# Optimization experiments

Measured on AMD Instinct MI355X. Metric: run time of the kernel, lower is better.

## Reference

```python
import jax, jax.numpy as jnp
import numpy as np

N_NODES = 100000
N_EDGES = 1600000
F_IN = 128
HID = 128  # nhid*2
NHID = 64
N_GRAPHS = 512
N_CLASSES = 10
NEG_SLOPE = 0.2  # PyG GATConv default


def setup_inputs() -> dict:
    key = jax.random.key(0)
    ks = jax.random.split(key, 16)
    x = jax.random.normal(ks[0], (N_NODES, F_IN), dtype=jnp.float32)
    edge_index = jax.random.randint(ks[1], (2, N_EDGES), 0, N_NODES, dtype=jnp.int64)
    batch = jnp.sort(jax.random.randint(ks[2], (N_NODES,), 0, N_GRAPHS, dtype=jnp.int64))
    def lin(k, fan_in, shape):
        bound = 1.0 / np.sqrt(fan_in)
        return jax.random.uniform(k, shape, jnp.float32, -bound, bound)
    return {
        "x": x, "edge_index": edge_index, "batch": batch,
        "W1": lin(ks[3], F_IN, (F_IN, HID)),
        "a_src1": lin(ks[4], HID, (HID,)),
        "a_dst1": lin(ks[5], HID, (HID,)),
        "b1": jnp.zeros((HID,), jnp.float32),
        "W2": lin(ks[6], HID, (HID, HID)),
        "a_src2": lin(ks[7], HID, (HID,)),
        "a_dst2": lin(ks[8], HID, (HID,)),
        "b2": jnp.zeros((HID,), jnp.float32),
        "W_fc1": lin(ks[9], HID, (HID, NHID)),
        "b_fc1": lin(ks[10], HID, (NHID,)),
        "W_fc2": lin(ks[11], NHID, (NHID, N_CLASSES)),
        "b_fc2": lin(ks[12], NHID, (N_CLASSES,)),
    }


def gat_conv(x, src, dst, W, a_src, a_dst, b):
    # h = W x ; attention e_ij = LeakyReLU(a_src.h_i + a_dst.h_j), softmax over
    # incoming edges of each destination j, then scatter-add aggregation.
    h = x @ W                                   # [N, H]
    alpha_s = h @ a_src                         # [N]
    alpha_d = h @ a_dst                         # [N]
    e = jax.nn.leaky_relu(alpha_s[src] + alpha_d[dst], NEG_SLOPE)  # [E]
    n = x.shape[0]
    m = jax.ops.segment_max(e, dst, num_segments=n)                # per-dst max
    ex = jnp.exp(e - m[dst])
    denom = jax.ops.segment_sum(ex, dst, num_segments=n)
    alpha = ex / denom[dst]                                        # [E]
    out = jax.ops.segment_sum(alpha[:, None] * h[src], dst, num_segments=n)
    return out + b


def reference(x, edge_index, batch, W1, a_src1, a_dst1, b1,
              W2, a_src2, a_dst2, b2, W_fc1, b_fc1, W_fc2, b_fc2):
    n = x.shape[0]
    # GATConv default add_self_loops=True
    loops = jnp.arange(n, dtype=edge_index.dtype)
    src = jnp.concatenate([edge_index[0], loops])
    dst = jnp.concatenate([edge_index[1], loops])

    h = jax.nn.selu(gat_conv(x, src, dst, W1, a_src1, a_dst1, b1))
    h = jax.nn.selu(gat_conv(h, src, dst, W2, a_src2, a_dst2, b2))

    # global mean pool over graphs
    sums = jax.ops.segment_sum(h, batch, num_segments=N_GRAPHS)
    cnts = jax.ops.segment_sum(jnp.ones((n,), h.dtype), batch, num_segments=N_GRAPHS)
    pooled = jax.nn.selu(sums / jnp.maximum(cnts, 1.0)[:, None])   # [G, H]

    g = jax.nn.selu(pooled @ W_fc1 + b_fc1)
    # dropout p=0.5 is identity in eval mode
    logits = g @ W_fc2 + b_fc2
    return jax.nn.log_softmax(logits, axis=-1)
```

## Files before the change

### kernel.cpp

```cpp
#include <hip/hip_runtime.h>
#include <hip/hip_bf16.h>

#define NEG_SLOPE 0.2f
typedef unsigned int uint32;

#define BSHIFT 9
#define BSIZE 512
#define MAXB 256
#define PCHUNK 2048
#define PEPT 8
#define BSTRIDE 12288

typedef __attribute__((ext_vector_type(8))) __bf16 bf16x8;
typedef __attribute__((ext_vector_type(4))) float f32x4;
typedef __attribute__((ext_vector_type(2))) float f32x2;

__device__ __forceinline__ float selu_f(float x) {
    const float a = 1.6732632423543772f, s = 1.0507009873554805f;
    return x > 0.0f ? s * x : s * a * (__expf(x) - 1.0f);
}

__device__ __forceinline__ unsigned short f2bf(float x) {
    uint32 u = __float_as_uint(x);
    uint32 r = (u + 0x7fff + ((u >> 16) & 1)) >> 16;
    return (unsigned short)r;
}
__device__ __forceinline__ float bf_lo(uint32 g) { return __uint_as_float(g << 16); }
__device__ __forceinline__ float bf_hi(uint32 g) { return __uint_as_float(g & 0xffff0000u); }

__global__ __launch_bounds__(256) void prep9(const float* __restrict__ W1,
                                             const float* __restrict__ W2,
                                             unsigned short* __restrict__ Wb,
                                             const int* __restrict__ batch,
                                             int* __restrict__ gstart,
                                             int N, int G) {
    int b = blockIdx.x, t = threadIdx.x;
    if (b < 2) {
        const float* W = b ? W2 : W1;
        unsigned short* oh = Wb + (size_t)b * 32768;
        unsigned short* ol = oh + 16384;
        for (int d = t; d < 16384; d += 256) {
            int j = d & 7, nn = (d >> 3) & 127, g = d >> 10;
            float v = W[(g * 8 + j) * 128 + nn];
            uint32 hu = f2bf(v);
            float hv = __uint_as_float(hu << 16);
            oh[d] = (unsigned short)hu;
            ol[d] = f2bf(v - hv);
        }
    } else {
        int i = (b - 2) * 256 + t;
        if (i < N) {
            int bb = batch[i];
            int bp = (i == 0) ? -1 : batch[i - 1];
            for (int q = bp + 1; q <= bb; ++q) gstart[q] = i;
            if (i == N - 1)
                for (int q = bb + 1; q <= G; ++q) gstart[q] = N;
        }
    }
}

__global__ __launch_bounds__(256) void partition_edges(const int* __restrict__ ei,
                                                       int* __restrict__ gcur0,
                                                       uint32* __restrict__ tmp,
                                                       int E, int TOT) {
    __shared__ int lcnt[MAXB];
    __shared__ int lstart[MAXB];
    __shared__ int lcur[MAXB];
    __shared__ int gbase[MAXB];
    __shared__ uint32 staged[PCHUNK];
    __shared__ unsigned char bslot[PCHUNK];
    int t = threadIdx.x;
    int eb = blockIdx.x * PCHUNK;
    int sreg[PEPT], dreg[PEPT];
    #pragma unroll
    for (int k = 0; k < PEPT; ++k) {
        int e = eb + k * 256 + t;
        if (e < TOT) {
            if (e < E) { sreg[k] = ei[e]; dreg[k] = ei[E + e]; }
            else       { sreg[k] = dreg[k] = e - E; }
        } else dreg[k] = -1;
    }
    lcnt[t] = 0;
    __syncthreads();
    #pragma unroll
    for (int k = 0; k < PEPT; ++k)
        if (dreg[k] >= 0) atomicAdd(&lcnt[dreg[k] >> BSHIFT], 1);
    __syncthreads();
    int v = lcnt[t];
    lstart[t] = v;
    __syncthreads();
    for (int off = 1; off < 256; off <<= 1) {
        int add = (t >= off) ? lstart[t - off] : 0;
        __syncthreads();
        lstart[t] += add;
        __syncthreads();
    }
    int ex = lstart[t] - v;
    __syncthreads();
    lstart[t] = ex;
    lcur[t] = ex;
    if (v > 0) gbase[t] = t * BSTRIDE + atomicAdd(&gcur0[t], v);
    __syncthreads();
    #pragma unroll
    for (int k = 0; k < PEPT; ++k) {
        int d = dreg[k];
        if (d >= 0) {
            int b = d >> BSHIFT;
            int p = atomicAdd(&lcur[b], 1);
            staged[p] = ((uint32)(d & (BSIZE - 1)) << 17) | (uint32)sreg[k];
            bslot[p] = (unsigned char)b;
        }
    }
    __syncthreads();
    int nvalid = TOT - eb; if (nvalid > PCHUNK) nvalid = PCHUNK;
    for (int i = t; i < nvalid; i += 256) {
        int b = bslot[i];
        tmp[gbase[b] + (i - lstart[b])] = staged[i];
    }
}

__global__ __launch_bounds__(1024) void bucket_build(const uint32* __restrict__ tmp,
                                                     const int* __restrict__ gcur0,
                                                     int* __restrict__ rowptr,
                                                     int* __restrict__ rowend,
                                                     int* __restrict__ col,
                                                     int N, int NB) {
    __shared__ int cnt[BSIZE];
    __shared__ int sums[256];
    int b = blockIdx.x, t = threadIdx.x;
    int lo = b << BSHIFT;
    int nn = N - lo; if (nn > BSIZE) nn = BSIZE;
    if (t < BSIZE) cnt[t] = 0;
    __syncthreads();
    int ebeg = b * BSTRIDE;
    int eend = ebeg + gcur0[b];
    for (int i = ebeg + t; i < eend; i += 1024)
        atomicAdd(&cnt[tmp[i] >> 17], 1);
    __syncthreads();
    int c0 = 0, c1 = 0, s2 = 0;
    if (t < 256) {
        c0 = cnt[2 * t]; c1 = cnt[2 * t + 1];
        s2 = c0 + c1;
        sums[t] = s2;
    }
    __syncthreads();
    for (int off = 1; off < 256; off <<= 1) {
        int add = (t < 256 && t >= off) ? sums[t - off] : 0;
        __syncthreads();
        if (t < 256) sums[t] += add;
        __syncthreads();
    }
    if (t < 256) {
        int ex = sums[t] - s2;
        int st0 = ebeg + ex, st1 = st0 + c0;
        if (2 * t < nn)     { rowptr[lo + 2 * t] = st0;     rowend[lo + 2 * t] = st0 + c0; }
        if (2 * t + 1 < nn) { rowptr[lo + 2 * t + 1] = st1; rowend[lo + 2 * t + 1] = st1 + c1; }
        cnt[2 * t] = st0; cnt[2 * t + 1] = st1;
    }
    __syncthreads();
    for (int i = ebeg + t; i < eend; i += 1024) {
        uint32 u = tmp[i];
        int p = atomicAdd(&cnt[u >> 17], 1);
        col[p] = (int)(u & 0x1FFFFu);
    }
}

__device__ __forceinline__ void gemm_core(const bf16x8 ah[2][4],
                                          const __bf16* Wl,
                                          const float* a_src, const float* a_dst,
                                          uint32* hb, float* as_, float* ad_,
                                          int rbase, int n, int col16, int quad) {
    f32x4 acc[2][8];
    #pragma unroll
    for (int mt = 0; mt < 2; ++mt)
        #pragma unroll
        for (int t = 0; t < 8; ++t) acc[mt][t] = (f32x4)(0.0f);

    #pragma unroll
    for (int c = 0; c < 4; ++c) {
        #pragma unroll
        for (int t = 0; t < 8; ++t) {
            int off = (((c * 4 + quad) * 128) + t * 16 + col16) * 8;
            bf16x8 bh = *(const bf16x8*)&Wl[off];
            bf16x8 bl = *(const bf16x8*)&Wl[16384 + off];
            #pragma unroll
            for (int mt = 0; mt < 2; ++mt) {
                acc[mt][t] = __builtin_amdgcn_mfma_f32_16x16x32_bf16(ah[mt][c], bh, acc[mt][t], 0, 0, 0);
                acc[mt][t] = __builtin_amdgcn_mfma_f32_16x16x32_bf16(ah[mt][c], bl, acc[mt][t], 0, 0, 0);
            }
        }
    }
    float asv[8], adv[8];
    #pragma unroll
    for (int t = 0; t < 8; ++t) { asv[t] = a_src[t * 16 + col16]; adv[t] = a_dst[t * 16 + col16]; }
    #pragma unroll
    for (int mt = 0; mt < 2; ++mt) {
        #pragma unroll
        for (int reg = 0; reg < 4; ++reg) {
            float s = 0.0f, d = 0.0f;
            #pragma unroll
            for (int t = 0; t < 8; ++t) {
                float v = acc[mt][t][reg];
                s += v * asv[t]; d += v * adv[t];
            }
            #pragma unroll
            for (int off = 1; off < 16; off <<= 1) {
                s += __shfl_xor(s, off);
                d += __shfl_xor(d, off);
            }
            int r = rbase + mt * 16 + quad * 4 + reg;
            if (col16 == 0 && r < n) { as_[r] = s; ad_[r] = d; }
        }
    }
    #pragma unroll
    for (int mt = 0; mt < 2; ++mt)
    #pragma unroll
    for (int t = 0; t < 8; ++t)
    #pragma unroll
    for (int reg = 0; reg < 4; ++reg) {
        float v = acc[mt][t][reg];
        float p = __shfl_xor(v, 1);
        int r = rbase + mt * 16 + quad * 4 + reg;
        if (!(col16 & 1) && r < n) {
            uint32 pk = (uint32)f2bf(v) | ((uint32)f2bf(p) << 16);
            hb[(size_t)r * 64 + t * 8 + (col16 >> 1)] = pk;
        }
    }
}

__global__ __launch_bounds__(256) void gemm_mfma_f32(const float* __restrict__ X,
                                                     const unsigned short* __restrict__ Wbh,
                                                     const float* __restrict__ a_src,
                                                     const float* __restrict__ a_dst,
                                                     uint32* __restrict__ hb,
                                                     float* __restrict__ as_,
                                                     float* __restrict__ ad_, int n) {
    __shared__ __bf16 Wl[32768];
    const int tid = threadIdx.x;
    {
        const uint4* sw = (const uint4*)Wbh;
        uint4* dw = (uint4*)Wl;
        for (int i = tid; i < 4096; i += 256) dw[i] = sw[i];
    }
    const int lane = tid & 63, wid = tid >> 6;
    const int col16 = lane & 15, quad = lane >> 4;
    const int rbase = blockIdx.x * 128 + wid * 32;
    bf16x8 ah[2][4];
    #pragma unroll
    for (int mt = 0; mt < 2; ++mt) {
        int r = rbase + mt * 16 + col16;
        bool ok = (r < n);
        const float* xp = X + (size_t)r * 128;
        #pragma unroll
        for (int c = 0; c < 4; ++c) {
            int k0 = c * 32 + quad * 8;
            float4 x0 = ok ? *(const float4*)(xp + k0)     : make_float4(0.f,0.f,0.f,0.f);
            float4 x1 = ok ? *(const float4*)(xp + k0 + 4) : make_float4(0.f,0.f,0.f,0.f);
            float xs[8] = {x0.x,x0.y,x0.z,x0.w,x1.x,x1.y,x1.z,x1.w};
            #pragma unroll
            for (int j = 0; j < 8; ++j) ah[mt][c][j] = (__bf16)xs[j];
        }
    }
    __syncthreads();
    gemm_core(ah, Wl, a_src, a_dst, hb, as_, ad_, rbase, n, col16, quad);
}

__global__ __launch_bounds__(256) void gemm_mfma_bf16(const __bf16* __restrict__ X,
                                                      const unsigned short* __restrict__ Wbh,
                                                      const float* __restrict__ a_src,
                                                      const float* __restrict__ a_dst,
                                                      uint32* __restrict__ hb,
                                                      float* __restrict__ as_,
                                                      float* __restrict__ ad_, int n) {
    __shared__ __bf16 Wl[32768];
    const int tid = threadIdx.x;
    {
        const uint4* sw = (const uint4*)Wbh;
        uint4* dw = (uint4*)Wl;
        for (int i = tid; i < 4096; i += 256) dw[i] = sw[i];
    }
    const int lane = tid & 63, wid = tid >> 6;
    const int col16 = lane & 15, quad = lane >> 4;
    const int rbase = blockIdx.x * 128 + wid * 32;
    bf16x8 ah[2][4];
    const bf16x8 zz = (bf16x8)((__bf16)0.0f);
    #pragma unroll
    for (int mt = 0; mt < 2; ++mt) {
        int r = rbase + mt * 16 + col16;
        bool ok = (r < n);
        const __bf16* xp = X + (size_t)r * 128;
        #pragma unroll
        for (int c = 0; c < 4; ++c)
            ah[mt][c] = ok ? *(const bf16x8*)(xp + c * 32 + quad * 8) : zz;
    }
    __syncthreads();
    gemm_core(ah, Wl, a_src, a_dst, hb, as_, ad_, rbase, n, col16, quad);
}

__global__ __launch_bounds__(256) void gat_csr4(const int* __restrict__ rowptr,
                                                const int* __restrict__ rowend,
                                                const int* __restrict__ col,
                                                const uint4* __restrict__ hb4,
                                                const float* __restrict__ as_,
                                                const float* __restrict__ ad_,
                                                const float* __restrict__ bias,
                                                uint4* __restrict__ outb, int n) {
    __shared__ float wsh[4][4][32];
    __shared__ int   ssh[4][4][32];
    const int wid = threadIdx.x >> 6;
    const int lane = threadIdx.x & 63;
    const int q = lane >> 4, l = lane & 15;
    const int node = blockIdx.x * 16 + wid * 4 + q;
    const bool valid = node < n;
    int beg = 0, end = 0;
    if (valid) { beg = rowptr[node]; end = rowend[node]; }
    float add = valid ? ad_[node] : 0.0f;
    int deg = end - beg;
    int m1 = max(deg, __shfl_xor(deg, 16));
    int mdeg = max(m1, __shfl_xor(m1, 32));
    float s = 0.0f;
    f32x2 ac[4];
    #pragma unroll
    for (int p = 0; p < 4; ++p) ac[p] = (f32x2)(0.0f);

    for (int cb = 0; cb < mdeg; cb += 32) {
        int j0 = beg + cb + l, j1 = j0 + 16;
        bool e0 = (j0 < end), e1 = (j1 < end);
        int s0 = e0 ? col[j0] : 0;
        int s1 = e1 ? col[j1] : 0;
        float v0 = as_[s0] + add;
        float v1 = as_[s1] + add;
        v0 = (v0 > 0.0f) ? v0 : NEG_SLOPE * v0;
        v1 = (v1 > 0.0f) ? v1 : NEG_SLOPE * v1;
        float w0 = e0 ? __expf(v0) : 0.0f;
        float w1 = e1 ? __expf(v1) : 0.0f;
        float ws = w0 + w1;
        #pragma unroll
        for (int off = 8; off > 0; off >>= 1) ws += __shfl_xor(ws, off);
        s += ws;
        wsh[wid][q][l] = w0;       wsh[wid][q][l + 16] = w1;
        ssh[wid][q][l] = s0;       ssh[wid][q][l + 16] = s1;

        int cnt = end - beg - cb;
        cnt = (cnt > 32) ? 32 : (cnt < 0 ? 0 : cnt);
        int t = 0;
        for (; t + 4 <= cnt; t += 4) {
            int sr[4]; float wr[4]; uint4 g[4];
            #pragma unroll
            for (int k = 0; k < 4; ++k) { sr[k] = ssh[wid][q][t + k]; wr[k] = wsh[wid][q][t + k]; }
            #pragma unroll
            for (int k = 0; k < 4; ++k) g[k] = hb4[(uint32)sr[k] * 16u + l];
            #pragma unroll
            for (int k = 0; k < 4; ++k) {
                f32x2 wv = (f32x2)wr[k];
                f32x2 u0 = { bf_lo(g[k].x), bf_hi(g[k].x) };
                f32x2 u1 = { bf_lo(g[k].y), bf_hi(g[k].y) };
                f32x2 u2 = { bf_lo(g[k].z), bf_hi(g[k].z) };
                f32x2 u3 = { bf_lo(g[k].w), bf_hi(g[k].w) };
                ac[0] = __builtin_elementwise_fma(wv, u0, ac[0]);
                ac[1] = __builtin_elementwise_fma(wv, u1, ac[1]);
                ac[2] = __builtin_elementwise_fma(wv, u2, ac[2]);
                ac[3] = __builtin_elementwise_fma(wv, u3, ac[3]);
            }
        }
        for (; t < cnt; ++t) {
            int sn = ssh[wid][q][t];
            float wt = wsh[wid][q][t];
            uint4 g = hb4[(uint32)sn * 16u + l];
            f32x2 wv = (f32x2)wt;
            f32x2 u0 = { bf_lo(g.x), bf_hi(g.x) };
            f32x2 u1 = { bf_lo(g.y), bf_hi(g.y) };
            f32x2 u2 = { bf_lo(g.z), bf_hi(g.z) };
            f32x2 u3 = { bf_lo(g.w), bf_hi(g.w) };
            ac[0] = __builtin_elementwise_fma(wv, u0, ac[0]);
            ac[1] = __builtin_elementwise_fma(wv, u1, ac[1]);
            ac[2] = __builtin_elementwise_fma(wv, u2, ac[2]);
            ac[3] = __builtin_elementwise_fma(wv, u3, ac[3]);
        }
    }
    if (valid) {
        float inv = 1.0f / s;
        float4 b0 = *(const float4*)&bias[l * 8];
        float4 b1 = *(const float4*)&bias[l * 8 + 4];
        float r0 = selu_f(ac[0].x * inv + b0.x);
        float r1 = selu_f(ac[0].y * inv + b0.y);
        float r2 = selu_f(ac[1].x * inv + b0.z);
        float r3 = selu_f(ac[1].y * inv + b0.w);
        float r4 = selu_f(ac[2].x * inv + b1.x);
        float r5 = selu_f(ac[2].y * inv + b1.y);
        float r6 = selu_f(ac[3].x * inv + b1.z);
        float r7 = selu_f(ac[3].y * inv + b1.w);
        uint4 o;
        o.x = (uint32)f2bf(r0) | ((uint32)f2bf(r1) << 16);
        o.y = (uint32)f2bf(r2) | ((uint32)f2bf(r3) << 16);
        o.z = (uint32)f2bf(r4) | ((uint32)f2bf(r5) << 16);
        o.w = (uint32)f2bf(r6) | ((uint32)f2bf(r7) << 16);
        outb[(uint32)node * 16u + l] = o;
    }
}

__global__ __launch_bounds__(128) void pool_head(const uint32* __restrict__ act,
                                                 const int* __restrict__ gstart,
                                                 const float* __restrict__ Wfc1,
                                                 const float* __restrict__ bfc1,
                                                 const float* __restrict__ Wfc2,
                                                 const float* __restrict__ bfc2,
                                                 float* __restrict__ out) {
    __shared__ float part[128][2];
    __shared__ float p[128];
    __shared__ float q[64];
    __shared__ float l[10];
    __shared__ float red[2];
    int g = blockIdx.x, t = threadIdx.x;
    int lo = gstart[g], hi = gstart[g + 1];
    int half = t >> 6, u = t & 63;
    float acc0 = 0.f, acc1 = 0.f;
    for (int nd = lo + half; nd < hi; nd += 2) {
        uint32 gv = act[(uint32)nd * 64u + u];
        acc0 += bf_lo(gv); acc1 += bf_hi(gv);
    }
    part[t][0] = acc0; part[t][1] = acc1;
    __syncthreads();
    if (half == 0) {
        float c = fmaxf((float)(hi - lo), 1.0f);
        p[2 * u]     = selu_f((acc0 + part[t + 64][0]) / c);
        p[2 * u + 1] = selu_f((acc1 + part[t + 64][1]) / c);
    }
    __syncthreads();
    if (t < 64) {
        float a = bfc1[t];
        #pragma unroll 8
        for (int k = 0; k < 128; ++k) a += p[k] * Wfc1[k * 64 + t];
        q[t] = selu_f(a);
    }
    __syncthreads();
    if (t < 10) {
        float a = bfc2[t];
        #pragma unroll
        for (int k = 0; k < 64; ++k) a += q[k] * Wfc2[k * 10 + t];
        l[t] = a;
    }
    __syncthreads();
    if (t == 0) {
        float mx = l[0];
        for (int c = 1; c < 10; ++c) mx = fmaxf(mx, l[c]);
        float sum = 0.0f;
        for (int c = 0; c < 10; ++c) sum += __expf(l[c] - mx);
        red[0] = mx; red[1] = logf(sum);
    }
    __syncthreads();
    if (t < 10) out[g * 10 + t] = l[t] - red[0] - red[1];
}

extern "C" void kernel_launch(void* const* d_in, const int* in_sizes, int n_in,
                              void* d_out, int out_size, void* d_ws, size_t ws_size,
                              hipStream_t stream) {
    const float* x      = (const float*)d_in[0];
    const int*   ei     = (const int*)d_in[1];
    const int*   batch  = (const int*)d_in[2];
    const float* W1     = (const float*)d_in[3];
    const float* asrc1  = (const float*)d_in[4];
    const float* adst1  = (const float*)d_in[5];
    const float* b1     = (const float*)d_in[6];
    const float* W2     = (const float*)d_in[7];
    const float* asrc2  = (const float*)d_in[8];
    const float* adst2  = (const float*)d_in[9];
    const float* b2     = (const float*)d_in[10];
    const float* Wfc1   = (const float*)d_in[11];
    const float* bfc1   = (const float*)d_in[12];
    const float* Wfc2   = (const float*)d_in[13];
    const float* bfc2   = (const float*)d_in[14];
    float* out = (float*)d_out;

    const int N = in_sizes[0] / 128;
    const int E = in_sizes[1] / 2;
    const int G = out_size / 10;
    const int TOT = E + N;
    const int NB = ((N - 1) >> BSHIFT) + 1;
    const int GB = (N + 255) / 256;
    const int PH = (TOT + PCHUNK - 1) / PCHUNK;
    const int GemmG = (N + 127) / 128;

    uint32* hb    = (uint32*)d_ws;
    uint32* h2b   = hb + (size_t)N * 64;
    uint32* tmp   = h2b + (size_t)N * 64;
    int*    col   = (int*)(tmp + (size_t)NB * BSTRIDE);
    float* as_    = (float*)(col + (size_t)NB * BSTRIDE);
    float* ad_    = as_ + N;
    int*   gstart = (int*)(ad_ + N);
    int*   rowptr = gstart + (G + 2);
    int*   rowend = rowptr + (N + 2);
    int*   gcur0  = rowend + (N + 2);
    unsigned short* Wb = (unsigned short*)(((uintptr_t)(gcur0 + MAXB) + 255) & ~(uintptr_t)255);

    const int gatGrid = (N + 15) / 16;

    hipMemsetAsync(gcur0, 0, MAXB * 4, stream);
    prep9<<<2 + GB, 256, 0, stream>>>(W1, W2, Wb, batch, gstart, N, G);
    partition_edges<<<PH, 256, 0, stream>>>(ei, gcur0, tmp, E, TOT);
    bucket_build<<<NB, 1024, 0, stream>>>(tmp, gcur0, rowptr, rowend, col, N, NB);

    gemm_mfma_f32<<<GemmG, 256, 0, stream>>>(x, Wb, asrc1, adst1, hb, as_, ad_, N);
    gat_csr4<<<gatGrid, 256, 0, stream>>>(rowptr, rowend, col, (const uint4*)hb, as_, ad_, b1, (uint4*)h2b, N);

    gemm_mfma_bf16<<<GemmG, 256, 0, stream>>>((const __bf16*)h2b, Wb + 32768, asrc2, adst2, hb, as_, ad_, N);
    gat_csr4<<<gatGrid, 256, 0, stream>>>(rowptr, rowend, col, (const uint2*)hb ? (const uint4*)hb : (const uint4*)hb, as_, ad_, b2, (uint4*)h2b, N);

    pool_head<<<G, 128, 0, stream>>>(h2b, gstart, Wfc1, bfc1, Wfc2, bfc2, out);
}
```

Before: 399.4 us.

## Double-buffer neighbor gathers in GAT aggregation using shuffles instead of LDS

Result: no change. 398.8 us (-0.1%).

```diff
diff --git a/kernel.cpp b/kernel.cpp
--- a/kernel.cpp
+++ b/kernel.cpp
@@ -297,7 +297,34 @@
     gemm_core(ah, Wl, a_src, a_dst, hb, as_, ad_, rbase, n, col16, quad);
 }
 
-__global__ __launch_bounds__(256) void gat_csr4(const int* __restrict__ rowptr,
+#define GIDX8(SARR, T0) { _Pragma("unroll") \
+    for (int k_ = 0; k_ < 8; ++k_) { int t_ = (T0) + k_; \
+        int sv_ = (t_ < 16) ? s0 : s1; \
+        int si_ = __shfl(sv_, base + (t_ & 15)); \
+        SARR[k_] = (t_ < cnt) ? si_ : 0; } }
+
+#define GLOAD8(GARR, SARR) { _Pragma("unroll") \
+    for (int k_ = 0; k_ < 8; ++k_) GARR[k_] = hb4[(uint32)SARR[k_] * 16u + l]; }
+
+#define GW8(WARR, T0) { _Pragma("unroll") \
+    for (int k_ = 0; k_ < 8; ++k_) { int t_ = (T0) + k_; \
+        float wv_ = (t_ < 16) ? w0 : w1; \
+        float wf_ = __shfl(wv_, base + (t_ & 15)); \
+        WARR[k_] = (t_ < cnt) ? wf_ : 0.0f; } }
+
+#define GCONSUME(GARR, WARR) { _Pragma("unroll") \
+    for (int k_ = 0; k_ < 8; ++k_) { \
+        f32x2 wv_ = (f32x2)WARR[k_]; \
+        f32x2 u0_ = { bf_lo(GARR[k_].x), bf_hi(GARR[k_].x) }; \
+        f32x2 u1_ = { bf_lo(GARR[k_].y), bf_hi(GARR[k_].y) }; \
+        f32x2 u2_ = { bf_lo(GARR[k_].z), bf_hi(GARR[k_].z) }; \
+        f32x2 u3_ = { bf_lo(GARR[k_].w), bf_hi(GARR[k_].w) }; \
+        ac[0] = __builtin_elementwise_fma(wv_, u0_, ac[0]); \
+        ac[1] = __builtin_elementwise_fma(wv_, u1_, ac[1]); \
+        ac[2] = __builtin_elementwise_fma(wv_, u2_, ac[2]); \
+        ac[3] = __builtin_elementwise_fma(wv_, u3_, ac[3]); } }
+
+__global__ __launch_bounds__(256) void gat_csr5(const int* __restrict__ rowptr,
                                                 const int* __restrict__ rowend,
                                                 const int* __restrict__ col,
                                                 const uint4* __restrict__ hb4,
@@ -305,11 +332,10 @@
                                                 const float* __restrict__ ad_,
                                                 const float* __restrict__ bias,
                                                 uint4* __restrict__ outb, int n) {
-    __shared__ float wsh[4][4][32];
-    __shared__ int   ssh[4][4][32];
     const int wid = threadIdx.x >> 6;
     const int lane = threadIdx.x & 63;
     const int q = lane >> 4, l = lane & 15;
+    const int base = lane & 48;
     const int node = blockIdx.x * 16 + wid * 4 + q;
     const bool valid = node < n;
     int beg = 0, end = 0;
@@ -328,6 +354,15 @@
         bool e0 = (j0 < end), e1 = (j1 < end);
         int s0 = e0 ? col[j0] : 0;
         int s1 = e1 ? col[j1] : 0;
+        int cnt = end - beg - cb;
+        cnt = (cnt < 0) ? 0 : (cnt > 32 ? 32 : cnt);
+        int rem = mdeg - cb; if (rem > 32) rem = 32;
+        const int NB8 = (rem + 7) >> 3;
+
+        int si[8]; uint4 gA[8], gB[8]; float wA[8], wB[8];
+
+        GIDX8(si, 0); GLOAD8(gA, si);
+
         float v0 = as_[s0] + add;
         float v1 = as_[s1] + add;
         v0 = (v0 > 0.0f) ? v0 : NEG_SLOPE * v0;
@@ -338,44 +373,19 @@
         #pragma unroll
         for (int off = 8; off > 0; off >>= 1) ws += __shfl_xor(ws, off);
         s += ws;
-        wsh[wid][q][l] = w0;       wsh[wid][q][l + 16] = w1;
-        ssh[wid][q][l] = s0;       ssh[wid][q][l + 16] = s1;
-
-        int cnt = end - beg - cb;
-        cnt = (cnt > 32) ? 32 : (cnt < 0 ? 0 : cnt);
-        int t = 0;
-        for (; t + 4 <= cnt; t += 4) {
-            int sr[4]; float wr[4]; uint4 g[4];
-            #pragma unroll
-            for (int k = 0; k < 4; ++k) { sr[k] = ssh[wid][q][t + k]; wr[k] = wsh[wid][q][t + k]; }
-            #pragma unroll
-            for (int k = 0; k < 4; ++k) g[k] = hb4[(uint32)sr[k] * 16u + l];
-            #pragma unroll
-            for (int k = 0; k < 4; ++k) {
-                f32x2 wv = (f32x2)wr[k];
-                f32x2 u0 = { bf_lo(g[k].x), bf_hi(g[k].x) };
-                f32x2 u1 = { bf_lo(g[k].y), bf_hi(g[k].y) };
-                f32x2 u2 = { bf_lo(g[k].z), bf_hi(g[k].z) };
-                f32x2 u3 = { bf_lo(g[k].w), bf_hi(g[k].w) };
-                ac[0] = __builtin_elementwise_fma(wv, u0, ac[0]);
-                ac[1] = __builtin_elementwise_fma(wv, u1, ac[1]);
-                ac[2] = __builtin_elementwise_fma(wv, u2, ac[2]);
-                ac[3] = __builtin_elementwise_fma(wv, u3, ac[3]);
-            }
-        }
-        for (; t < cnt; ++t) {
-            int sn = ssh[wid][q][t];
-            float wt = wsh[wid][q][t];
-            uint4 g = hb4[(uint32)sn * 16u + l];
-            f32x2 wv = (f32x2)wt;
-            f32x2 u0 = { bf_lo(g.x), bf_hi(g.x) };
-            f32x2 u1 = { bf_lo(g.y), bf_hi(g.y) };
-            f32x2 u2 = { bf_lo(g.z), bf_hi(g.z) };
-            f32x2 u3 = { bf_lo(g.w), bf_hi(g.w) };
-            ac[0] = __builtin_elementwise_fma(wv, u0, ac[0]);
-            ac[1] = __builtin_elementwise_fma(wv, u1, ac[1]);
-            ac[2] = __builtin_elementwise_fma(wv, u2, ac[2]);
-            ac[3] = __builtin_elementwise_fma(wv, u3, ac[3]);
+        GW8(wA, 0);
+
+        int b = 0;
+        while (true) {
+            bool moreB = (b + 1 < NB8);
+            if (moreB) { GIDX8(si, (b + 1) * 8); GLOAD8(gB, si); GW8(wB, (b + 1) * 8); }
+            GCONSUME(gA, wA);
+            if (!moreB) break;
+            bool moreA = (b + 2 < NB8);
+            if (moreA) { GIDX8(si, (b + 2) * 8); GLOAD8(gA, si); GW8(wA, (b + 2) * 8); }
+            GCONSUME(gB, wB);
+            if (!moreA) break;
+            b += 2;
         }
     }
     if (valid) {
@@ -501,10 +511,10 @@
     bucket_build<<<NB, 1024, 0, stream>>>(tmp, gcur0, rowptr, rowend, col, N, NB);
 
     gemm_mfma_f32<<<GemmG, 256, 0, stream>>>(x, Wb, asrc1, adst1, hb, as_, ad_, N);
-    gat_csr4<<<gatGrid, 256, 0, stream>>>(rowptr, rowend, col, (const uint4*)hb, as_, ad_, b1, (uint4*)h2b, N);
+    gat_csr5<<<gatGrid, 256, 0, stream>>>(rowptr, rowend, col, (const uint4*)hb, as_, ad_, b1, (uint4*)h2b, N);
 
     gemm_mfma_bf16<<<GemmG, 256, 0, stream>>>((const __bf16*)h2b, Wb + 32768, asrc2, adst2, hb, as_, ad_, N);
-    gat_csr4<<<gatGrid, 256, 0, stream>>>(rowptr, rowend, col, (const uint2*)hb ? (const uint4*)hb : (const uint4*)hb, as_, ad_, b2, (uint4*)h2b, N);
+    gat_csr5<<<gatGrid, 256, 0, stream>>>(rowptr, rowend, col, (const uint4*)hb, as_, ad_, b2, (uint4*)h2b, N);
 
     pool_head<<<G, 128, 0, stream>>>(h2b, gstart, Wfc1, bfc1, Wfc2, bfc2, out);
 }
```
